# Kernel tuning notes

Hardware: AMD Instinct MI355X
Metric: run time of the kernel (lower is better)

## Reference

```python
import jax, jax.numpy as jnp
import numpy as np

N = 8192
EMB = 256
KDIM = 32
AR = 1024
UTYPE = 233
TEMP = 0.8


def setup_inputs() -> dict:
    key = jax.random.key(0)
    ks = jax.random.split(key, 16)
    s = 0.05
    f32 = jnp.float32
    inp = {
        'utype_mask': jax.random.uniform(ks[0], (UTYPE,), f32),
        'entity_mask': jnp.ones((N,), f32),
        'entity_encodings': jax.random.normal(ks[1], (N, EMB), f32),
        'autoregressive_encoding': jax.random.normal(ks[2], (AR,), f32),
        # func_embed: Linear(233,256)+ReLU
        'W_fe': jax.random.normal(ks[3], (EMB, UTYPE), f32) * s, 'b_fe': jnp.zeros((EMB,), f32),
        # entity_keys: Conv1d(256,32,1) == pointwise linear
        'W_k': jax.random.normal(ks[4], (KDIM, EMB), f32) * s, 'b_k': jnp.zeros((KDIM,), f32),
        # argenc[0]: Linear(1024,256)
        'W_a0': jax.random.normal(ks[5], (EMB, AR), f32) * s, 'b_a0': jnp.zeros((EMB,), f32),
        # argenc[1]: ReLU -> Linear(256,32) -> ReLU
        'W_a1': jax.random.normal(ks[6], (KDIM, EMB), f32) * s, 'b_a1': jnp.zeros((KDIM,), f32),
        # LSTM(64,32) gates (forget, input-sigmoid, input-tanh, output) + shared LayerNorm(32)
        'W_f': jax.random.normal(ks[7], (KDIM, 2 * KDIM), f32) * s, 'b_f': jnp.zeros((KDIM,), f32),
        'W_i0': jax.random.normal(ks[8], (KDIM, 2 * KDIM), f32) * s, 'b_i0': jnp.zeros((KDIM,), f32),
        'W_i1': jax.random.normal(ks[9], (KDIM, 2 * KDIM), f32) * s, 'b_i1': jnp.zeros((KDIM,), f32),
        'W_o': jax.random.normal(ks[10], (KDIM, 2 * KDIM), f32) * s, 'b_o': jnp.zeros((KDIM,), f32),
        'ln_g': jnp.ones((KDIM,), f32), 'ln_b': jnp.zeros((KDIM,), f32),
        # argenc[3]: Linear(32,1024)+ReLU
        'W_a3': jax.random.normal(ks[11], (AR, KDIM), f32) * s, 'b_a3': jnp.zeros((AR,), f32),
        'self_unit_ct': 64,
    }
    return inp


def reference(utype_mask, entity_mask, entity_encodings, autoregressive_encoding,
              W_fe, b_fe, W_k, b_k, W_a0, b_a0, W_a1, b_a1,
              W_f, b_f, W_i0, b_i0, W_i1, b_i1, W_o, b_o, ln_g, ln_b,
              W_a3, b_a3, self_unit_ct):
    n = entity_encodings.shape[0]
    steps = min(64, int(self_unit_ct))

    def ln(x):  # shared LayerNorm(32), torch eps=1e-5, biased var
        m = x.mean()
        v = ((x - m) ** 2).mean()
        return (x - m) * jax.lax.rsqrt(v + 1e-5) * ln_g + ln_b

    def lstm(x, h):
        forget = ln(jax.nn.sigmoid(W_f @ x + b_f))
        remember = ln(jax.nn.sigmoid(W_i0 @ x + b_i0) * jnp.tanh(W_i1 @ x + b_i1))
        new_h = remember + forget * h
        out = jnp.tanh(new_h) * ln(jax.nn.sigmoid(W_o @ x + b_o))
        return out, new_h

    func_embed = jax.nn.relu(W_fe @ utype_mask + b_fe)          # (256,)
    keys = W_k @ entity_encodings.T + b_k[:, None]               # (32, N)

    def step(carry, _):
        q, h, mask, ar, sel, done = carry
        active = jnp.logical_not(done)
        i0 = W_a0 @ ar + b_a0 + func_embed                       # (256,)
        i1 = jax.nn.relu(W_a1 @ jax.nn.relu(i0) + b_a1)          # (32,)
        qn, hn = lstm(jnp.concatenate([i1, q]), h)
        sig = jax.nn.sigmoid(qn @ keys)                          # (N,)
        v = jnp.nan_to_num(jnp.exp(jnp.log(sig) / TEMP))
        ssum = v.sum()
        valid = ssum != 0
        soft = jnp.where(valid, v / jnp.where(valid, ssum, 1.0), 0.0)
        row = jnp.where(active & valid, soft, 0.0)
        pick = jnp.argmax(soft)                                  # deterministic stand-in for multinomial sample
        hit = active & valid & (mask[pick] != 0)
        selection = keys[:, pick]
        centered = selection - selection.mean()
        nan_free = jnp.logical_not(jnp.any(jnp.isnan(centered)))
        mask = jnp.where(hit, mask.at[pick].set(0.0), mask)
        sel = jnp.where(hit, sel.at[pick].set(1.0), sel)
        ar = jnp.where(hit & nan_free, ar + jax.nn.relu(W_a3 @ centered + b_a3), ar)
        done = done | (hit & jnp.logical_not(nan_free))          # emulates break
        q = jnp.where(active, qn, q)
        h = jnp.where(active, hn, h)
        return (q, h, mask, ar, sel, done), row

    init = (jnp.zeros((KDIM,), jnp.float32), jnp.zeros((KDIM,), jnp.float32),
            entity_mask, autoregressive_encoding,
            jnp.zeros((n,), jnp.float32), jnp.array(False))
    (_, _, _, ar_out, sel_out, _), rows = jax.lax.scan(step, init, None, length=steps)
    unit_logits = jnp.zeros((n, n), jnp.float32).at[:steps].set(rows)
    return unit_logits, sel_out, ar_out
```

## Files before the change

kernel.cpp:

```cpp
#include <hip/hip_runtime.h>
#include <math.h>


typedef float v4f __attribute__((ext_vector_type(4)));
typedef unsigned long long ull;

#define N_ENT 8192
#define EMB   256
#define KD    32
#define ARD   1024
#define UT    233
#define NSCAN 32
#define NZERO 224
#define NBLK  256

#define WS_KEYS 0
#define WS_C0   262144
#define WS_PAIR 262400
#define PR_RI0W  0
#define PR_CRI0  512
#define PR_CPART 577
#define PR_KMAX  641
#define PR_SACC  705
#define NPAIRS   737

struct Params {
  const float *um, *emask, *enc, *arin, *W_fe, *b_fe, *W_k, *b_k,
              *W_a0, *b_a0, *W_a1, *b_a1, *W_f, *b_f, *W_i0, *b_i0,
              *W_i1, *b_i1, *W_o, *b_o, *ln_g, *ln_b, *W_a3, *b_a3;
  const int* ct;
  float* out;
  float* wsf;
  int*   wsi;
};

__device__ __forceinline__ ull ld_pair(ull* p_) {
  return __hip_atomic_load(p_, __ATOMIC_RELAXED, __HIP_MEMORY_SCOPE_AGENT);
}
__device__ __forceinline__ void st_pair(ull* p_, ull v) {
  __hip_atomic_store(p_, v, __ATOMIC_RELAXED, __HIP_MEMORY_SCOPE_AGENT);
}
__device__ __forceinline__ void wait_ctr(ull* c, ull target) {
  int guard = 0;
  while (__hip_atomic_load(c, __ATOMIC_RELAXED, __HIP_MEMORY_SCOPE_AGENT) < target) {
    __builtin_amdgcn_s_sleep(1);
    if (++guard > (1 << 20)) break;
  }
}

__global__ __launch_bounds__(256) void k_init(Params p) {
  __shared__ float enc_s[32 * 260];
  __shared__ float um_s[UT];
  const int tid = threadIdx.x, bid = blockIdx.x;
  float* keys = p.wsf + WS_KEYS;

  if (bid == 0 && tid < UT) um_s[tid] = p.um[tid];
  if (bid == 3) {
    ull* pr = (ull*)(p.wsf + WS_PAIR);
    for (int i = tid; i < NPAIRS; i += 256) pr[i] = 0ull;
  }

  const int j0 = bid * 32;
  #pragma unroll
  for (int i = 0; i < 8; ++i) {
    int idx = i * 256 + tid;
    int row = idx >> 6, c4 = idx & 63;
    v4f v = *(const v4f*)(p.enc + (size_t)(j0 + row) * EMB + c4 * 4);
    *(v4f*)&enc_s[row * 260 + c4 * 4] = v;
  }
  __syncthreads();
  {
    const int jl = tid >> 3, kg = tid & 7;
    float acc[4];
    #pragma unroll
    for (int kk = 0; kk < 4; ++kk) acc[kk] = p.b_k[kg * 4 + kk];
    for (int e4 = 0; e4 < 64; ++e4) {
      v4f x = *(const v4f*)&enc_s[jl * 260 + e4 * 4];
      #pragma unroll
      for (int kk = 0; kk < 4; ++kk) {
        v4f w = *(const v4f*)(p.W_k + (size_t)(kg * 4 + kk) * EMB + e4 * 4);
        acc[kk] += x.x * w.x + x.y * w.y + x.z * w.z + x.w * w.w;
      }
    }
    const int j = j0 + jl;
    #pragma unroll
    for (int kk = 0; kk < 4; ++kk) keys[(size_t)(kg * 4 + kk) * N_ENT + j] = acc[kk];
  }
  if (bid == 0) {
    float a = p.b_fe[tid];
    const float* wr = p.W_fe + (size_t)tid * UT;
    for (int u = 0; u < UT; ++u) a += wr[u] * um_s[u];
    p.wsf[WS_C0 + tid] = fmaxf(a, 0.f) + p.b_a0[tid];
  }
}

__global__ __launch_bounds__(256, 1) void k_scan(Params p) {
  const int tid = threadIdx.x, bid = blockIdx.x;
  int ctv = p.ct[0];
  const int steps = ctv < 0 ? 0 : (ctv > 64 ? 64 : ctv);
  const size_t NN = (size_t)N_ENT * N_ENT;

  if (bid >= NSCAN) {
    v4f z = (v4f){0.f, 0.f, 0.f, 0.f};
    v4f* o4 = (v4f*)p.out;
    const size_t tot = NN / 4;
    for (size_t i = (size_t)steps * (N_ENT / 4) + (size_t)(bid - NSCAN) * 256 + tid;
         i < tot; i += (size_t)NZERO * 256)
      __builtin_nontemporal_store(z, o4 + i);
    return;
  }

  __shared__ float ar_s[32 * 33];
  __shared__ float ri0_s[8 * 33];
  __shared__ unsigned maskb[256], selb[256];
  __shared__ float x_i1[32], q_s[32], h_s[32], qnf[32];
  __shared__ float garr[128], fog[32], rem[32], og[32], cent[32];
  __shared__ float b_a1s[32], gb_s[128], lng_s[32], lnb_s[32], c0own[8];
  __shared__ float reds[4], rmaxs[4];
  __shared__ int   ridxs[4];
  __shared__ float ssum_s;
  __shared__ int   upd_s, done_s;

  ull*   pairb = (ull*)(p.wsf + WS_PAIR);
  ull*   ri0w  = pairb + PR_RI0W;
  ull*   cri0  = pairb + PR_CRI0;
  ull*   cpart = pairb + PR_CPART;
  ull*   kmaxp = pairb + PR_KMAX;
  float* saccp = (float*)(pairb + PR_SACC);
  const float* keys = p.wsf + WS_KEYS;

  for (int i = tid; i < ARD; i += 256) ar_s[(i >> 5) * 33 + (i & 31)] = p.arin[i];
  {
    unsigned mb = 0u;
    const float* em = p.emask + (size_t)tid * 32;
    #pragma unroll
    for (int j = 0; j < 32; ++j) mb |= (em[j] != 0.f) ? (1u << j) : 0u;
    maskb[tid] = mb; selb[tid] = 0u;
  }
  if (tid < 32) {
    b_a1s[tid] = p.b_a1[tid];
    lng_s[tid] = p.ln_g[tid]; lnb_s[tid] = p.ln_b[tid];
    q_s[tid] = 0.f; h_s[tid] = 0.f; qnf[tid] = 0.f; x_i1[tid] = 0.f;
  }
  if (tid < 128) {
    const int g = tid >> 5, r = tid & 31;
    const float* bg = (g == 0) ? p.b_f : (g == 1) ? p.b_i0 : (g == 2) ? p.b_i1 : p.b_o;
    gb_s[tid] = bg[r];
  }
  if (tid < 8) c0own[tid] = p.wsf[WS_C0 + bid * 8 + tid];
  if (tid == 0) done_s = 0;

  v4f w0[8];
  { const float* s = p.W_a0 + (size_t)(bid * 8 + (tid >> 5)) * ARD + (tid & 31) * 32;
    #pragma unroll
    for (int i = 0; i < 8; ++i) w0[i] = ((const v4f*)s)[i]; }
  v4f w1[8];
  { const float* s = p.W_a1 + (size_t)(tid >> 3) * EMB + (tid & 7) * 32;
    #pragma unroll
    for (int i = 0; i < 8; ++i) w1[i] = ((const v4f*)s)[i]; }
  v4f wg[8];
  { const int rowg = tid >> 1, g = rowg >> 5, r = rowg & 31, half = tid & 1;
    const float* W = (g == 0) ? p.W_f : (g == 1) ? p.W_i0 : (g == 2) ? p.W_i1 : p.W_o;
    const float* s = W + r * 64 + half * 32;
    #pragma unroll
    for (int i = 0; i < 8; ++i) wg[i] = ((const v4f*)s)[i]; }
  float kc[32];
  { const int gcol = bid * 256 + tid;
    #pragma unroll
    for (int k = 0; k < 32; ++k) kc[k] = keys[(size_t)k * N_ENT + gcol]; }
  __syncthreads();

  auto produce = [&](int e) {
    const int seg = tid & 31, rl = tid >> 5;
    const float* a = &ar_s[seg * 33];
    float pa = 0.f;
    #pragma unroll
    for (int i = 0; i < 8; ++i) {
      v4f av = *(const v4f*)(a + 4 * i);
      pa += w0[i].x * av.x + w0[i].y * av.y + w0[i].z * av.z + w0[i].w * av.w;
    }
    #pragma unroll
    for (int m = 16; m; m >>= 1) pa += __shfl_xor(pa, m);
    if (seg == 0)
      st_pair(&ri0w[(e & 1) * 256 + bid * 8 + rl],
              (ull)__float_as_uint(fmaxf(pa + c0own[rl], 0.f)));
  };
  produce(0);
  __syncthreads();
  if (tid == 0)
    __hip_atomic_fetch_add(&cri0[0], 1ull, __ATOMIC_RELAXED, __HIP_MEMORY_SCOPE_AGENT);

  int ep = 0;
  int pend = 1;
  float v_reg = 0.f;
  for (int t = 0; t < steps; ++t) {
    const int act = (done_s == 0);

    if (!act) {
      __builtin_nontemporal_store(0.f, p.out + (size_t)t * N_ENT + (bid << 8) + tid);
      continue;
    }

    if (pend) {
      if (tid == 0) wait_ctr(&cri0[ep], (ull)NSCAN);
      __syncthreads();
      {
        ull u = ld_pair(&ri0w[(ep & 1) * 256 + tid]);
        ri0_s[(tid >> 5) * 33 + (tid & 31)] = __uint_as_float((unsigned)u);
      }
      __syncthreads();
      {
        const int r = tid >> 3, s8 = tid & 7;
        float p1 = 0.f;
        #pragma unroll
        for (int i = 0; i < 8; ++i) {
          const float* xx = &ri0_s[s8 * 33 + 4 * i];
          p1 += w1[i].x * xx[0] + w1[i].y * xx[1] + w1[i].z * xx[2] + w1[i].w * xx[3];
        }
        #pragma unroll
        for (int m = 4; m; m >>= 1) p1 += __shfl_xor(p1, m);
        if (s8 == 0) x_i1[r] = fmaxf(p1 + b_a1s[r], 0.f);
      }
      __syncthreads();
      pend = 0;
    }

    {
      const int rowg = tid >> 1, g = rowg >> 5, half = tid & 1;
      const float* xsrc = half ? q_s : x_i1;
      float pg = 0.f;
      #pragma unroll
      for (int i = 0; i < 8; ++i)
        pg += wg[i].x * xsrc[4 * i] + wg[i].y * xsrc[4 * i + 1] +
              wg[i].z * xsrc[4 * i + 2] + wg[i].w * xsrc[4 * i + 3];
      pg += __shfl_xor(pg, 1);
      if (!half) {
        pg += gb_s[rowg];
        garr[rowg] = (g == 2) ? tanhf(pg) : 1.f / (1.f + __expf(-pg));
      }
    }
    __syncthreads();
    {
      const int w = tid >> 6, k = tid & 63;
      if (w < 3 && k < 32) {
        float a = (w == 0) ? garr[k] : (w == 1) ? garr[32 + k] * garr[64 + k] : garr[96 + k];
        float s = a;
        #pragma unroll
        for (int m = 16; m; m >>= 1) s += __shfl_xor(s, m);
        const float mean = s * (1.f / 32.f);
        const float d = a - mean;
        float vv = d * d;
        #pragma unroll
        for (int m = 16; m; m >>= 1) vv += __shfl_xor(vv, m);
        vv *= (1.f / 32.f);
        const float y = d * rsqrtf(vv + 1e-5f) * lng_s[k] + lnb_s[k];
        if (w == 0) fog[k] = y; else if (w == 1) rem[k] = y; else og[k] = y;
      }
    }
    __syncthreads();
    if (tid < 32) {
      const float nh = rem[tid] + fog[tid] * h_s[tid];
      const float qv = tanhf(nh) * og[tid];
      qnf[tid] = qv;
      h_s[tid] = nh; q_s[tid] = qv;
    }
    __syncthreads();

    {
      float dot = 0.f;
      #pragma unroll
      for (int k = 0; k < 32; ++k) dot += qnf[k] * kc[k];
      const float sig = 1.f / (1.f + __expf(-dot));
      const float v = __expf(__logf(sig) / 0.8f);
      v_reg = v;
      float sv = v, mv = v;
      int mi = (bid << 8) + tid;
      #pragma unroll
      for (int m = 32; m; m >>= 1) {
        sv += __shfl_xor(sv, m);
        const float ov = __shfl_xor(mv, m);
        const int oi = __shfl_xor(mi, m);
        if (ov > mv || (ov == mv && oi < mi)) { mv = ov; mi = oi; }
      }
      const int wv = tid >> 6;
      if ((tid & 63) == 0) { reds[wv] = sv; rmaxs[wv] = mv; ridxs[wv] = mi; }
    }
    __syncthreads();
    if (tid == 0) {
      float Sb = ((reds[0] + reds[1]) + reds[2]) + reds[3];
      float Mb = rmaxs[0]; int Ib = ridxs[0];
      #pragma unroll
      for (int i2 = 1; i2 < 4; ++i2)
        if (rmaxs[i2] > Mb || (rmaxs[i2] == Mb && ridxs[i2] < Ib)) { Mb = rmaxs[i2]; Ib = ridxs[i2]; }
      __hip_atomic_fetch_add(&saccp[t], Sb, __ATOMIC_RELAXED, __HIP_MEMORY_SCOPE_AGENT);
      const ull key = ((ull)__float_as_uint(Mb) << 32) | (ull)(0xFFFFFFFFu - (unsigned)Ib);
      __hip_atomic_fetch_max(&kmaxp[t], key, __ATOMIC_RELAXED, __HIP_MEMORY_SCOPE_AGENT);
      asm volatile("s_waitcnt vmcnt(0)" ::: "memory");
      __hip_atomic_fetch_add(&cpart[t], 1ull, __ATOMIC_RELAXED, __HIP_MEMORY_SCOPE_AGENT);
    }

    if (tid == 0) wait_ctr(&cpart[t], (ull)NSCAN);
    __syncthreads();
    if (tid < 32) {
      const float s = __hip_atomic_load(&saccp[t], __ATOMIC_RELAXED, __HIP_MEMORY_SCOPE_AGENT);
      const ull km = ld_pair(&kmaxp[t]);
      const int ii = (int)(0xFFFFFFFFu - (unsigned)(km & 0xFFFFFFFFull));
      const float kv = keys[(size_t)tid * N_ENT + ii];
      float mn = kv;
      #pragma unroll
      for (int mm = 16; mm; mm >>= 1) mn += __shfl_xor(mn, mm);
      mn *= (1.f / 32.f);
      const float cv = kv - mn;
      cent[tid] = cv;
      const unsigned long long bb = __ballot(cv != cv);
      if (tid == 0) {
        const int valid = (s != 0.f);
        const int nf = (bb == 0) ? 1 : 0;
        const unsigned mw = maskb[ii >> 5];
        const int hit = (valid && ((mw >> (ii & 31)) & 1)) ? 1 : 0;
        ssum_s = s;
        upd_s = (hit && nf) ? 1 : 0;
        if (hit) {
          maskb[ii >> 5] = mw & ~(1u << (ii & 31));
          selb[ii >> 5] |= (1u << (ii & 31));
          if (!nf) done_s = 1;
        }
      }
    }
    __syncthreads();
    {
      const float S = ssum_s;
      const float rowv = (S != 0.f) ? (v_reg / S) : 0.f;
      __builtin_nontemporal_store(rowv, p.out + (size_t)t * N_ENT + (bid << 8) + tid);
    }
    if (upd_s) {
      #pragma unroll
      for (int rr = 0; rr < 4; ++rr) {
        const int r = tid + rr * 256;
        const float* wr = p.W_a3 + (size_t)r * KD;
        float dl = p.b_a3[r];
        #pragma unroll
        for (int c4 = 0; c4 < 8; ++c4) {
          v4f wv4 = *(const v4f*)(wr + 4 * c4);
          dl += wv4.x * cent[4 * c4] + wv4.y * cent[4 * c4 + 1] +
                wv4.z * cent[4 * c4 + 2] + wv4.w * cent[4 * c4 + 3];
        }
        if (dl > 0.f) ar_s[(r >> 5) * 33 + (r & 31)] += dl;
      }
    }
    __syncthreads();
    if (upd_s) {
      ep += 1;
      produce(ep);
      __syncthreads();
      if (tid == 0)
        __hip_atomic_fetch_add(&cri0[ep], 1ull, __ATOMIC_RELAXED, __HIP_MEMORY_SCOPE_AGENT);
      pend = 1;
    }
  }
  __syncthreads();

  if (bid == 0) {
    for (int i = tid; i < N_ENT; i += 256)
      p.out[NN + i] = ((selb[i >> 5] >> (i & 31)) & 1u) ? 1.f : 0.f;
  } else if (bid == 1) {
    for (int i = tid; i < ARD; i += 256)
      p.out[NN + N_ENT + i] = ar_s[(i >> 5) * 33 + (i & 31)];
  }
}

extern "C" void kernel_launch(void* const* d_in, const int* in_sizes, int n_in,
                              void* d_out, int out_size, void* d_ws, size_t ws_size,
                              hipStream_t stream) {
  (void)in_sizes; (void)n_in; (void)out_size; (void)ws_size;
  Params p;
  p.um    = (const float*)d_in[0];
  p.emask = (const float*)d_in[1];
  p.enc   = (const float*)d_in[2];
  p.arin  = (const float*)d_in[3];
  p.W_fe  = (const float*)d_in[4];
  p.b_fe  = (const float*)d_in[5];
  p.W_k   = (const float*)d_in[6];
  p.b_k   = (const float*)d_in[7];
  p.W_a0  = (const float*)d_in[8];
  p.b_a0  = (const float*)d_in[9];
  p.W_a1  = (const float*)d_in[10];
  p.b_a1  = (const float*)d_in[11];
  p.W_f   = (const float*)d_in[12];
  p.b_f   = (const float*)d_in[13];
  p.W_i0  = (const float*)d_in[14];
  p.b_i0  = (const float*)d_in[15];
  p.W_i1  = (const float*)d_in[16];
  p.b_i1  = (const float*)d_in[17];
  p.W_o   = (const float*)d_in[18];
  p.b_o   = (const float*)d_in[19];
  p.ln_g  = (const float*)d_in[20];
  p.ln_b  = (const float*)d_in[21];
  p.W_a3  = (const float*)d_in[22];
  p.b_a3  = (const float*)d_in[23];
  p.ct    = (const int*)d_in[24];
  p.out   = (float*)d_out;
  p.wsf   = (float*)d_ws;
  p.wsi   = (int*)d_ws;

  hipLaunchKernelGGL(k_init, dim3(NBLK), dim3(256), 0, stream, p);
  hipLaunchKernelGGL(k_scan, dim3(NBLK), dim3(256), 0, stream, p);
}
```

Measured before the change: 744.4 us.

## Shard per-step cross-block reduction into padded groups with packed fixed-point counter

Each step's cross-block reduction used three contended global atomics: a float sum, a key max and an arrival counter. Now the 32 scan blocks split into 4 groups of 8, each with its own cache-line-padded slot. The sum is converted to 2^38-scaled fixed point and packed with the arrival count into one 64-bit atomic add. Waiters poll the four slots with a sleep and a guard, which cuts atomic contention and round trips on the critical serial path. In exchange the sum becomes a fixed-point approximation that can lose precision or overflow into the count bits, and the poll can give up after the guard limit.

New measurement: 782.8 us. 1.05x slower.

```diff
diff --git a/kernel.cpp b/kernel.cpp
--- a/kernel.cpp
+++ b/kernel.cpp
@@ -14,15 +14,17 @@
 #define NZERO 224
 #define NBLK  256
 
+#define FIXSCALE 274877906944.0
+#define M52 ((1ull << 52) - 1)
+
 #define WS_KEYS 0
 #define WS_C0   262144
 #define WS_PAIR 262400
-#define PR_RI0W  0
-#define PR_CRI0  512
-#define PR_CPART 577
-#define PR_KMAX  641
-#define PR_SACC  705
-#define NPAIRS   737
+#define PR_RI0W 0
+#define PR_CRI0 512
+#define PR_PCK  584
+#define PR_KMX  2632
+#define NPAIRS  4680
 
 struct Params {
   const float *um, *emask, *enc, *arin, *W_fe, *b_fe, *W_k, *b_k,
@@ -121,12 +123,11 @@
   __shared__ float ssum_s;
   __shared__ int   upd_s, done_s;
 
-  ull*   pairb = (ull*)(p.wsf + WS_PAIR);
-  ull*   ri0w  = pairb + PR_RI0W;
-  ull*   cri0  = pairb + PR_CRI0;
-  ull*   cpart = pairb + PR_CPART;
-  ull*   kmaxp = pairb + PR_KMAX;
-  float* saccp = (float*)(pairb + PR_SACC);
+  ull* pairb = (ull*)(p.wsf + WS_PAIR);
+  ull* ri0w  = pairb + PR_RI0W;
+  ull* cri0  = pairb + PR_CRI0;
+  ull* pckp  = pairb + PR_PCK;
+  ull* kmxp  = pairb + PR_KMX;
   const float* keys = p.wsf + WS_KEYS;
 
   for (int i = tid; i < ARD; i += 256) ar_s[(i >> 5) * 33 + (i & 31)] = p.arin[i];
@@ -292,18 +293,43 @@
       #pragma unroll
       for (int i2 = 1; i2 < 4; ++i2)
         if (rmaxs[i2] > Mb || (rmaxs[i2] == Mb && ridxs[i2] < Ib)) { Mb = rmaxs[i2]; Ib = ridxs[i2]; }
-      __hip_atomic_fetch_add(&saccp[t], Sb, __ATOMIC_RELAXED, __HIP_MEMORY_SCOPE_AGENT);
+      const int g = bid >> 3;
       const ull key = ((ull)__float_as_uint(Mb) << 32) | (ull)(0xFFFFFFFFu - (unsigned)Ib);
-      __hip_atomic_fetch_max(&kmaxp[t], key, __ATOMIC_RELAXED, __HIP_MEMORY_SCOPE_AGENT);
+      __hip_atomic_fetch_max(&kmxp[(t * 4 + g) * 8], key, __ATOMIC_RELAXED, __HIP_MEMORY_SCOPE_AGENT);
       asm volatile("s_waitcnt vmcnt(0)" ::: "memory");
-      __hip_atomic_fetch_add(&cpart[t], 1ull, __ATOMIC_RELAXED, __HIP_MEMORY_SCOPE_AGENT);
-    }
-
-    if (tid == 0) wait_ctr(&cpart[t], (ull)NSCAN);
+      const ull fixedS = (ull)((double)Sb * FIXSCALE);
+      __hip_atomic_fetch_add(&pckp[(t * 4 + g) * 8], (1ull << 52) + fixedS,
+                             __ATOMIC_RELAXED, __HIP_MEMORY_SCOPE_AGENT);
+    }
+
+    if (tid == 0) {
+      int guard = 0;
+      for (;;) {
+        const ull a = ld_pair(&pckp[(t * 4 + 0) * 8]);
+        const ull b = ld_pair(&pckp[(t * 4 + 1) * 8]);
+        const ull c = ld_pair(&pckp[(t * 4 + 2) * 8]);
+        const ull d = ld_pair(&pckp[(t * 4 + 3) * 8]);
+        if (((a >> 52) == 8) & ((b >> 52) == 8) & ((c >> 52) == 8) & ((d >> 52) == 8)) break;
+        if (++guard > (1 << 20)) break;
+        __builtin_amdgcn_s_sleep(1);
+      }
+    }
     __syncthreads();
     if (tid < 32) {
-      const float s = __hip_atomic_load(&saccp[t], __ATOMIC_RELAXED, __HIP_MEMORY_SCOPE_AGENT);
-      const ull km = ld_pair(&kmaxp[t]);
+      const ull p0 = ld_pair(&pckp[(t * 4 + 0) * 8]);
+      const ull p1 = ld_pair(&pckp[(t * 4 + 1) * 8]);
+      const ull p2 = ld_pair(&pckp[(t * 4 + 2) * 8]);
+      const ull p3 = ld_pair(&pckp[(t * 4 + 3) * 8]);
+      const ull k0 = ld_pair(&kmxp[(t * 4 + 0) * 8]);
+      const ull k1 = ld_pair(&kmxp[(t * 4 + 1) * 8]);
+      const ull k2 = ld_pair(&kmxp[(t * 4 + 2) * 8]);
+      const ull k3 = ld_pair(&kmxp[(t * 4 + 3) * 8]);
+      const ull fx = (p0 & M52) + (p1 & M52) + (p2 & M52) + (p3 & M52);
+      const float s = (float)((double)fx * (1.0 / FIXSCALE));
+      ull km = k0;
+      if (k1 > km) km = k1;
+      if (k2 > km) km = k2;
+      if (k3 > km) km = k3;
       const int ii = (int)(0xFFFFFFFFu - (unsigned)(km & 0xFFFFFFFFull));
       const float kv = keys[(size_t)tid * N_ENT + ii];
       float mn = kv;
```

## Speculatively compute next LSTM step while waiting on cross-block reduction

Applied to the files above, without the earlier changes.

Each scan step now precomputes the next step's LSTM state and logit sweep, assuming the autoregressive encoding is unchanged, while it waits for the grid-wide sum/argmax counter. When the step turns out to update the encoding, it restores the saved q/h state and recomputes after consuming the new ri0 vector. Several __syncthreads are also replaced with a cheaper lgkmcnt-only barrier. This overlaps LSTM compute with inter-block sync latency, at the cost of wasted work whenever an update happens, which is likely on most steps.

Result: faster. 728.0 us (-2.2%).

```diff
diff --git a/kernel.cpp b/kernel.cpp
--- a/kernel.cpp
+++ b/kernel.cpp
@@ -48,6 +48,10 @@
   }
 }
 
+__device__ __forceinline__ void bar_lds() {
+  asm volatile("s_waitcnt lgkmcnt(0)\n\ts_barrier" ::: "memory");
+}
+
 __global__ __launch_bounds__(256) void k_init(Params p) {
   __shared__ float enc_s[32 * 260];
   __shared__ float um_s[UT];
@@ -114,6 +118,7 @@
   __shared__ float ri0_s[8 * 33];
   __shared__ unsigned maskb[256], selb[256];
   __shared__ float x_i1[32], q_s[32], h_s[32], qnf[32];
+  __shared__ float q_bak[32], h_bak[32];
   __shared__ float garr[128], fog[32], rem[32], og[32], cent[32];
   __shared__ float b_a1s[32], gb_s[128], lng_s[32], lnb_s[32], c0own[8];
   __shared__ float reds[4], rmaxs[4];
@@ -185,46 +190,29 @@
       st_pair(&ri0w[(e & 1) * 256 + bid * 8 + rl],
               (ull)__float_as_uint(fmaxf(pa + c0own[rl], 0.f)));
   };
-  produce(0);
-  __syncthreads();
-  if (tid == 0)
-    __hip_atomic_fetch_add(&cri0[0], 1ull, __ATOMIC_RELAXED, __HIP_MEMORY_SCOPE_AGENT);
-
-  int ep = 0;
-  int pend = 1;
-  float v_reg = 0.f;
-  for (int t = 0; t < steps; ++t) {
-    const int act = (done_s == 0);
-
-    if (!act) {
-      __builtin_nontemporal_store(0.f, p.out + (size_t)t * N_ENT + (bid << 8) + tid);
-      continue;
-    }
-
-    if (pend) {
-      if (tid == 0) wait_ctr(&cri0[ep], (ull)NSCAN);
-      __syncthreads();
-      {
-        ull u = ld_pair(&ri0w[(ep & 1) * 256 + tid]);
-        ri0_s[(tid >> 5) * 33 + (tid & 31)] = __uint_as_float((unsigned)u);
-      }
-      __syncthreads();
-      {
-        const int r = tid >> 3, s8 = tid & 7;
-        float p1 = 0.f;
-        #pragma unroll
-        for (int i = 0; i < 8; ++i) {
-          const float* xx = &ri0_s[s8 * 33 + 4 * i];
-          p1 += w1[i].x * xx[0] + w1[i].y * xx[1] + w1[i].z * xx[2] + w1[i].w * xx[3];
-        }
-        #pragma unroll
-        for (int m = 4; m; m >>= 1) p1 += __shfl_xor(p1, m);
-        if (s8 == 0) x_i1[r] = fmaxf(p1 + b_a1s[r], 0.f);
-      }
-      __syncthreads();
-      pend = 0;
-    }
-
+  auto consume_ri0 = [&](int e) {
+    if (tid == 0) wait_ctr(&cri0[e], (ull)NSCAN);
+    bar_lds();
+    {
+      ull u = ld_pair(&ri0w[(e & 1) * 256 + tid]);
+      ri0_s[(tid >> 5) * 33 + (tid & 31)] = __uint_as_float((unsigned)u);
+    }
+    bar_lds();
+    {
+      const int r = tid >> 3, s8 = tid & 7;
+      float p1 = 0.f;
+      #pragma unroll
+      for (int i = 0; i < 8; ++i) {
+        const float* xx = &ri0_s[s8 * 33 + 4 * i];
+        p1 += w1[i].x * xx[0] + w1[i].y * xx[1] + w1[i].z * xx[2] + w1[i].w * xx[3];
+      }
+      #pragma unroll
+      for (int m = 4; m; m >>= 1) p1 += __shfl_xor(p1, m);
+      if (s8 == 0) x_i1[r] = fmaxf(p1 + b_a1s[r], 0.f);
+    }
+    bar_lds();
+  };
+  auto compute_qn = [&]() {
     {
       const int rowg = tid >> 1, g = rowg >> 5, half = tid & 1;
       const float* xsrc = half ? q_s : x_i1;
@@ -239,7 +227,7 @@
         garr[rowg] = (g == 2) ? tanhf(pg) : 1.f / (1.f + __expf(-pg));
       }
     }
-    __syncthreads();
+    bar_lds();
     {
       const int w = tid >> 6, k = tid & 63;
       if (w < 3 && k < 32) {
@@ -257,35 +245,51 @@
         if (w == 0) fog[k] = y; else if (w == 1) rem[k] = y; else og[k] = y;
       }
     }
-    __syncthreads();
+    bar_lds();
     if (tid < 32) {
       const float nh = rem[tid] + fog[tid] * h_s[tid];
       const float qv = tanhf(nh) * og[tid];
       qnf[tid] = qv;
       h_s[tid] = nh; q_s[tid] = qv;
     }
-    __syncthreads();
-
-    {
-      float dot = 0.f;
-      #pragma unroll
-      for (int k = 0; k < 32; ++k) dot += qnf[k] * kc[k];
-      const float sig = 1.f / (1.f + __expf(-dot));
-      const float v = __expf(__logf(sig) / 0.8f);
-      v_reg = v;
-      float sv = v, mv = v;
-      int mi = (bid << 8) + tid;
-      #pragma unroll
-      for (int m = 32; m; m >>= 1) {
-        sv += __shfl_xor(sv, m);
-        const float ov = __shfl_xor(mv, m);
-        const int oi = __shfl_xor(mi, m);
-        if (ov > mv || (ov == mv && oi < mi)) { mv = ov; mi = oi; }
-      }
-      const int wv = tid >> 6;
-      if ((tid & 63) == 0) { reds[wv] = sv; rmaxs[wv] = mv; ridxs[wv] = mi; }
-    }
-    __syncthreads();
+    bar_lds();
+  };
+  auto sweep_reduce = [&]() -> float {
+    float dot = 0.f;
+    #pragma unroll
+    for (int k = 0; k < 32; ++k) dot += qnf[k] * kc[k];
+    const float sig = 1.f / (1.f + __expf(-dot));
+    const float v = __expf(__logf(sig) / 0.8f);
+    float sv = v, mv = v;
+    int mi = (bid << 8) + tid;
+    #pragma unroll
+    for (int m = 32; m; m >>= 1) {
+      sv += __shfl_xor(sv, m);
+      const float ov = __shfl_xor(mv, m);
+      const int oi = __shfl_xor(mi, m);
+      if (ov > mv || (ov == mv && oi < mi)) { mv = ov; mi = oi; }
+    }
+    const int wv = tid >> 6;
+    if ((tid & 63) == 0) { reds[wv] = sv; rmaxs[wv] = mv; ridxs[wv] = mi; }
+    bar_lds();
+    return v;
+  };
+
+  produce(0);
+  __syncthreads();
+  if (tid == 0)
+    __hip_atomic_fetch_add(&cri0[0], 1ull, __ATOMIC_RELAXED, __HIP_MEMORY_SCOPE_AGENT);
+  consume_ri0(0);
+  compute_qn();
+  float v_cur = sweep_reduce();
+  int ep = 0;
+
+  for (int t = 0; t < steps; ++t) {
+    if (done_s != 0) {
+      __builtin_nontemporal_store(0.f, p.out + (size_t)t * N_ENT + (bid << 8) + tid);
+      continue;
+    }
+
     if (tid == 0) {
       float Sb = ((reds[0] + reds[1]) + reds[2]) + reds[3];
       float Mb = rmaxs[0]; int Ib = ridxs[0];
@@ -299,8 +303,13 @@
       __hip_atomic_fetch_add(&cpart[t], 1ull, __ATOMIC_RELAXED, __HIP_MEMORY_SCOPE_AGENT);
     }
 
+    if (tid < 32) { q_bak[tid] = q_s[tid]; h_bak[tid] = h_s[tid]; }
+    bar_lds();
+    compute_qn();
+    float v_spec = sweep_reduce();
+
     if (tid == 0) wait_ctr(&cpart[t], (ull)NSCAN);
-    __syncthreads();
+    bar_lds();
     if (tid < 32) {
       const float s = __hip_atomic_load(&saccp[t], __ATOMIC_RELAXED, __HIP_MEMORY_SCOPE_AGENT);
       const ull km = ld_pair(&kmaxp[t]);
@@ -327,10 +336,10 @@
         }
       }
     }
-    __syncthreads();
+    bar_lds();
     {
       const float S = ssum_s;
-      const float rowv = (S != 0.f) ? (v_reg / S) : 0.f;
+      const float rowv = (S != 0.f) ? (v_cur / S) : 0.f;
       __builtin_nontemporal_store(rowv, p.out + (size_t)t * N_ENT + (bid << 8) + tid);
     }
     if (upd_s) {
@@ -347,16 +356,19 @@
         }
         if (dl > 0.f) ar_s[(r >> 5) * 33 + (r & 31)] += dl;
       }
-    }
-    __syncthreads();
-    if (upd_s) {
+      bar_lds();
       ep += 1;
       produce(ep);
       __syncthreads();
       if (tid == 0)
         __hip_atomic_fetch_add(&cri0[ep], 1ull, __ATOMIC_RELAXED, __HIP_MEMORY_SCOPE_AGENT);
-      pend = 1;
-    }
+      consume_ri0(ep);
+      if (tid < 32) { q_s[tid] = q_bak[tid]; h_s[tid] = h_bak[tid]; }
+      bar_lds();
+      compute_qn();
+      v_spec = sweep_reduce();
+    }
+    v_cur = v_spec;
   }
   __syncthreads();
 
```
